# Optimization experiments

Measured on AMD Instinct MI355X. Metric: run time of the kernel, lower is better.

## Reference

```python
import jax, jax.numpy as jnp
import numpy as np

B, T, D = 4, 1024, 1024
H = 16                      # attention heads
DS, DC, EXP = 16, 4, 2      # d_state, d_conv, expand
DIN = EXP * D               # 2048
DTR = D // 16               # dt_rank = 64
TOPK_RATIO = 0.25
EPS = 1e-5


def setup_inputs() -> dict:
    key = jax.random.key(0)
    ks = jax.random.split(key, 16)
    def n(k, shape, scale=0.02):
        return jax.random.normal(k, shape, jnp.float32) * scale
    return {
        "x": jax.random.normal(ks[0], (B, T, D), jnp.float32),
        "ln_w": jnp.ones((D,), jnp.float32),
        "ln_b": jnp.zeros((D,), jnp.float32),
        "r_w1": n(ks[1], (D, D // 2)),
        "r_b1": jnp.zeros((D // 2,), jnp.float32),
        "r_w2": n(ks[2], (D // 2, 1)),
        "r_b2": jnp.zeros((1,), jnp.float32),
        "Wq": n(ks[3], (D, D)), "bq": jnp.zeros((D,), jnp.float32),
        "Wk": n(ks[4], (D, D)), "bk": jnp.zeros((D,), jnp.float32),
        "Wv": n(ks[5], (D, D)), "bv": jnp.zeros((D,), jnp.float32),
        "Wo": n(ks[6], (D, D)), "bo": jnp.zeros((D,), jnp.float32),
        "in_w": n(ks[7], (D, 2 * DIN)),
        "conv_w": n(ks[8], (DIN, DC), 0.1),
        "conv_b": jnp.zeros((DIN,), jnp.float32),
        "xproj_w": n(ks[9], (DIN, DTR + 2 * DS)),
        "dt_w": n(ks[10], (DTR, DIN), 0.1),
        "dt_b": jnp.full((DIN,), -4.0, jnp.float32) + n(ks[11], (DIN,), 0.1),
        "A_log": jnp.log(jnp.broadcast_to(jnp.arange(1, DS + 1, dtype=jnp.float32), (DIN, DS))),
        "Dp": jnp.ones((DIN,), jnp.float32),
        "out_w": n(ks[12], (DIN, D)),
    }


def _attn_core(x, Wq, bq, Wk, bk, Wv, bv, Wo, bo):
    b, L, d = x.shape
    hd = d // H
    q = (x @ Wq + bq).reshape(b, L, H, hd)
    k = (x @ Wk + bk).reshape(b, L, H, hd)
    v = (x @ Wv + bv).reshape(b, L, H, hd)
    scores = jnp.einsum('bqhd,bkhd->bhqk', q, k) / jnp.sqrt(jnp.float32(hd))
    p = jax.nn.softmax(scores, axis=-1)
    o = jnp.einsum('bhqk,bkhd->bqhd', p, v).reshape(b, L, d)
    return o @ Wo + bo


def _ssm_core(u, in_w, conv_w, conv_b, xproj_w, dt_w, dt_b, A_log, Dp, out_w):
    # Mamba-style selective SSM on the sub-sequence u: (b, L, D)
    b, L, _ = u.shape
    xi, z = jnp.split(u @ in_w, 2, axis=-1)            # (b, L, DIN) each
    xp = jnp.pad(xi, ((0, 0), (DC - 1, 0), (0, 0)))    # causal depthwise conv1d
    xc = conv_b + sum(xp[:, j:j + L] * conv_w[:, j] for j in range(DC))
    xc = jax.nn.silu(xc)
    proj = xc @ xproj_w                                # (b, L, DTR + 2*DS)
    dtp = proj[..., :DTR]
    Bm = proj[..., DTR:DTR + DS]
    Cm = proj[..., DTR + DS:]
    delta = jax.nn.softplus(dtp @ dt_w + dt_b)         # (b, L, DIN)
    A = -jnp.exp(A_log)                                # (DIN, DS)
    dA = jnp.exp(delta[..., None] * A)                 # (b, L, DIN, DS)
    dBu = (delta * xc)[..., None] * Bm[:, :, None, :]  # (b, L, DIN, DS)

    def step(h, inp):
        dA_t, dBu_t, C_t = inp
        h = dA_t * h + dBu_t                           # (b, DIN, DS)
        return h, jnp.einsum('bds,bs->bd', h, C_t)

    xs = (jnp.moveaxis(dA, 1, 0), jnp.moveaxis(dBu, 1, 0), jnp.moveaxis(Cm, 1, 0))
    _, ys = jax.lax.scan(step, jnp.zeros((b, DIN, DS), u.dtype), xs)
    y = jnp.moveaxis(ys, 0, 1) + xc * Dp               # (b, L, DIN)
    y = y * jax.nn.silu(z)
    return y @ out_w


def reference(x, ln_w, ln_b, r_w1, r_b1, r_w2, r_b2, Wq, bq, Wk, bk, Wv, bv, Wo, bo,
              in_w, conv_w, conv_b, xproj_w, dt_w, dt_b, A_log, Dp, out_w):
    b, t, d = x.shape
    k = min(max(1, int(TOPK_RATIO * t)), t)            # static top-k count
    # pre-norm (LayerNorm)
    mu = x.mean(-1, keepdims=True)
    var = ((x - mu) ** 2).mean(-1, keepdims=True)
    xn = (x - mu) * jax.lax.rsqrt(var + EPS) * ln_w + ln_b
    # router scores (b, t) and top-k dispatch
    scores = jnp.squeeze(jax.nn.gelu(xn @ r_w1 + r_b1) @ r_w2 + r_b2, -1)
    _, topk_idx = jax.lax.top_k(scores, k)
    bidx = jnp.arange(b)[:, None]
    mask = jnp.zeros((b, t), bool).at[bidx, topk_idx].set(True)
    # unselected positions in ascending order (stable sort of 0/1 mask)
    order = jnp.argsort(mask.astype(jnp.int32), axis=1)
    bottom_idx = order[:, :t - k]
    # SSM branch on bottom (t-k) tokens, order-preserving
    x_ssm = xn[bidx, bottom_idx]                       # (b, t-k, d)
    d_ssm_tok = _ssm_core(x_ssm, in_w, conv_w, conv_b, xproj_w, dt_w, dt_b, A_log, Dp, out_w)
    delta_ssm = jnp.zeros_like(xn).at[bidx, bottom_idx].set(d_ssm_tok)
    # attention branch on top-k tokens only (sparse attention)
    x_attn = xn[bidx, topk_idx]                        # (b, k, d)
    d_attn_tok = _attn_core(x_attn, Wq, bq, Wk, bk, Wv, bv, Wo, bo)
    delta_attn = jnp.zeros_like(xn).at[bidx, topk_idx].set(d_attn_tok)
    # masked merge + residual
    delta = jnp.where(mask[..., None], delta_attn, delta_ssm)
    return x + delta
```

## Files before the change

### kernel.cpp

```cpp
#include <hip/hip_runtime.h>
#include <hip/hip_bf16.h>
#include <cstdint>
#include <cstddef>

typedef unsigned short u16;
typedef __attribute__((ext_vector_type(8))) short short8;
typedef __attribute__((ext_vector_type(4))) float f32x4;

__device__ __forceinline__ float b2f(u16 h){ union{unsigned u; float f;} c; c.u = ((unsigned)h)<<16; return c.f; }
__device__ __forceinline__ u16 f2b(float f){ union{float f; unsigned u;} c; c.f = f; unsigned u = c.u; return (u16)((u + 0x7fffu + ((u>>16)&1u)) >> 16); }
__device__ __forceinline__ float gelu_f(float x){
  float x3 = x*x*x;
  return 0.5f*x*(1.f + tanhf(0.7978845608028654f*(x + 0.044715f*x3)));
}
__device__ __forceinline__ void gload_lds16(const void* g, void* l){
  __builtin_amdgcn_global_load_lds((const __attribute__((address_space(1))) void*)g,
                                   (__attribute__((address_space(3))) void*)l, 16, 0, 0);
}

__global__ __launch_bounds__(256) void k_ln(const float* __restrict__ x, const float* __restrict__ w,
    const float* __restrict__ b, float* __restrict__ xn)
{
  int t = blockIdx.x; int tid = threadIdx.x;
  const float* xr = x + (size_t)t*1024;
  float v0 = xr[tid], v1 = xr[tid+256], v2 = xr[tid+512], v3 = xr[tid+768];
  __shared__ float red[256];
  red[tid] = v0+v1+v2+v3; __syncthreads();
  for (int o=128;o;o>>=1){ if (tid<o) red[tid]+=red[tid+o]; __syncthreads(); }
  float mu = red[0] * (1.f/1024.f);
  __syncthreads();
  float c0=v0-mu,c1=v1-mu,c2=v2-mu,c3=v3-mu;
  red[tid] = c0*c0+c1*c1+c2*c2+c3*c3; __syncthreads();
  for (int o=128;o;o>>=1){ if (tid<o) red[tid]+=red[tid+o]; __syncthreads(); }
  float inv = rsqrtf(red[0]*(1.f/1024.f) + 1e-5f);
  float* xo = xn + (size_t)t*1024;
  xo[tid]     = c0*inv*w[tid]     + b[tid];
  xo[tid+256] = c1*inv*w[tid+256] + b[tid+256];
  xo[tid+512] = c2*inv*w[tid+512] + b[tid+512];
  xo[tid+768] = c3*inv*w[tid+768] + b[tid+768];
}

__global__ __launch_bounds__(256) void k_tcvt(const float* __restrict__ src, u16* __restrict__ dst, int R, int C)
{
  __shared__ float tile[32][33];
  int c0 = blockIdx.x*32, r0 = blockIdx.y*32;
  int lc = threadIdx.x & 31, lr = threadIdx.x >> 5;
  #pragma unroll
  for (int rr=0; rr<4; rr++) tile[lr + rr*8][lc] = src[(size_t)(r0 + lr + rr*8)*C + c0 + lc];
  __syncthreads();
  #pragma unroll
  for (int rr=0; rr<4; rr++) dst[(size_t)(c0 + lr + rr*8)*R + r0 + lc] = f2b(tile[lc][lr + rr*8]);
}

__global__ __launch_bounds__(256) void k_bpack(const float* __restrict__ bq, const float* __restrict__ bk,
    const float* __restrict__ bv, float* __restrict__ o)
{
  int i = blockIdx.x*256 + threadIdx.x;
  o[i] = (i < 1024) ? bq[i] : ((i < 2048) ? bk[i-1024] : bv[i-2048]);
}

__global__ __launch_bounds__(256) void k_gemm_router(const float* __restrict__ A, const float* __restrict__ B,
    const float* __restrict__ bias, float* __restrict__ C, int K, int N)
{
  __shared__ float at[16][64];
  __shared__ float bt[16][68];
  int tid = threadIdx.x;
  int tm = blockIdx.x*64, tn = blockIdx.y*64;
  int tr = tid >> 4, tc = tid & 15;
  float acc[4][4] = {};
  for (int k0=0;k0<K;k0+=16){
    int arow = tid >> 2, ac4 = (tid & 3) * 4;
    float4 va = *(const float4*)&A[(size_t)(tm+arow)*K + k0 + ac4];
    at[ac4+0][arow]=va.x; at[ac4+1][arow]=va.y; at[ac4+2][arow]=va.z; at[ac4+3][arow]=va.w;
    int brow = tid >> 4, bc4 = (tid & 15) * 4;
    *(float4*)&bt[brow][bc4] = *(const float4*)&B[(size_t)(k0+brow)*N + tn + bc4];
    __syncthreads();
    #pragma unroll
    for (int kk=0;kk<16;kk++){
      float a0=at[kk][tr*4+0],a1=at[kk][tr*4+1],a2=at[kk][tr*4+2],a3=at[kk][tr*4+3];
      float b0=bt[kk][tc*4+0],b1=bt[kk][tc*4+1],b2v=bt[kk][tc*4+2],b3=bt[kk][tc*4+3];
      acc[0][0]+=a0*b0; acc[0][1]+=a0*b1; acc[0][2]+=a0*b2v; acc[0][3]+=a0*b3;
      acc[1][0]+=a1*b0; acc[1][1]+=a1*b1; acc[1][2]+=a1*b2v; acc[1][3]+=a1*b3;
      acc[2][0]+=a2*b0; acc[2][1]+=a2*b1; acc[2][2]+=a2*b2v; acc[2][3]+=a2*b3;
      acc[3][0]+=a3*b0; acc[3][1]+=a3*b1; acc[3][2]+=a3*b2v; acc[3][3]+=a3*b3;
    }
    __syncthreads();
  }
  #pragma unroll
  for (int i=0;i<4;i++)
    #pragma unroll
    for (int j=0;j<4;j++){
      int r = tm+tr*4+i, c = tn+tc*4+j;
      C[(size_t)r*N + c] = gelu_f(acc[i][j] + bias[c]);
    }
}

__global__ __launch_bounds__(256) void k_score(const float* __restrict__ h, const float* __restrict__ w2,
    const float* __restrict__ b2, float* __restrict__ scores)
{
  int tok = blockIdx.x*4 + (threadIdx.x >> 6);
  int lane = threadIdx.x & 63;
  const float* hr = h + (size_t)tok*512;
  float s = 0.f;
  #pragma unroll
  for (int i=0;i<8;i++) s += hr[lane + i*64] * w2[lane + i*64];
  #pragma unroll
  for (int o=32;o;o>>=1) s += __shfl_xor(s, o, 64);
  if (lane==0) scores[tok] = s + b2[0];
}

__global__ __launch_bounds__(1024) void k_topk(const float* __restrict__ scores, int* __restrict__ aidx, int* __restrict__ sidx)
{
  int b = blockIdx.x, tid = threadIdx.x;
  __shared__ float s[1024];
  __shared__ int pf[1024];
  s[tid] = scores[b*1024 + tid];
  __syncthreads();
  float my = s[tid];
  int cnt = 0;
  for (int j=0;j<1024;j++){ float sj = s[j]; cnt += (sj > my) || (sj == my && j < tid); }
  int isa = (cnt < 256) ? 1 : 0;
  pf[tid] = isa; __syncthreads();
  for (int o=1;o<1024;o<<=1){
    int add = (tid >= o) ? pf[tid-o] : 0;
    __syncthreads();
    pf[tid] += add;
    __syncthreads();
  }
  int excl = pf[tid] - isa;
  if (isa) aidx[b*256 + excl] = tid;
  else     sidx[b*768 + (tid - excl)] = tid;
}

__global__ __launch_bounds__(256) void k_gather(const float* __restrict__ xn, const int* __restrict__ aidx,
    const int* __restrict__ sidx, u16* __restrict__ xat, u16* __restrict__ xst)
{
  int id = blockIdx.x;
  int b = id >> 10, s = id & 1023;
  int src; u16* dst;
  if (s < 256) { src = aidx[b*256 + s]; dst = xat + (size_t)(b*256 + s)*1024; }
  else { int ss = s - 256; src = sidx[b*768 + ss]; dst = xst + (size_t)(b*768 + ss)*1024; }
  const float* sp = xn + ((size_t)b*1024 + src)*1024;
  int tid = threadIdx.x;
  dst[tid]     = f2b(sp[tid]);
  dst[tid+256] = f2b(sp[tid+256]);
  dst[tid+512] = f2b(sp[tid+512]);
  dst[tid+768] = f2b(sp[tid+768]);
}

template<int BM, int BN>
__global__ __launch_bounds__(256) void k_mfma(const u16* __restrict__ A, int lda,
    const u16* __restrict__ Bt, int ldb, const float* __restrict__ bias,
    float* __restrict__ outf, u16* __restrict__ outb, int M, int N, int K,
    int act, int split)
{
  constexpr int WTM = BM/2, WTN = BN/2;
  constexpr int MI = WTM/16, NJ = WTN/16;
  __shared__ u16 lA[2][BM*32];
  __shared__ u16 lB[2][BN*32];
  const int tid = threadIdx.x;
  const int lane = tid & 63;
  const int wv = tid >> 6;
  const int wm = wv >> 1, wn = wv & 1;
  const int tm = blockIdx.x * BM, tn = blockIdx.y * BN;
  const int r0 = lane & 15;
  const int kg = lane >> 4;

  const int ksl = K / gridDim.z;
  const int kbeg = blockIdx.z * ksl;
  if (gridDim.z > 1) outf += (size_t)blockIdx.z * ((size_t)M * N);

  auto stage = [&](int buf, int kt){
    for (int c = tid; c < BM*4; c += 256) {
      int row = c >> 2, j = c & 3;
      int jj = j ^ ((row >> 1) & 3);
      gload_lds16(&A[(size_t)(tm + row)*lda + kt + jj*8], &lA[buf][c*8]);
    }
    for (int c = tid; c < BN*4; c += 256) {
      int row = c >> 2, j = c & 3;
      int jj = j ^ ((row >> 1) & 3);
      gload_lds16(&Bt[(size_t)(tn + row)*ldb + kt + jj*8], &lB[buf][c*8]);
    }
  };

  f32x4 acc[MI][NJ];
  #pragma unroll
  for (int i=0;i<MI;i++)
    #pragma unroll
    for (int j=0;j<NJ;j++) acc[i][j] = (f32x4){0.f,0.f,0.f,0.f};

  stage(0, kbeg);
  __syncthreads();
  const int nk = ksl / 32;
  int cur = 0;
  for (int t = 0; t < nk; t++) {
    if (t + 1 < nk) stage(cur ^ 1, kbeg + (t+1)*32);
    short8 av[MI], bvv[NJ];
    #pragma unroll
    for (int i=0;i<MI;i++){
      int row = wm*WTM + i*16 + r0;
      av[i] = *(const short8*)&lA[cur][row*32 + ((kg ^ ((row>>1)&3))<<3)];
    }
    #pragma unroll
    for (int j=0;j<NJ;j++){
      int row = wn*WTN + j*16 + r0;
      bvv[j] = *(const short8*)&lB[cur][row*32 + ((kg ^ ((row>>1)&3))<<3)];
    }
    #pragma unroll
    for (int i=0;i<MI;i++)
      #pragma unroll
      for (int j=0;j<NJ;j++)
        acc[i][j] = __builtin_amdgcn_mfma_f32_16x16x32_bf16(av[i], bvv[j], acc[i][j], 0, 0, 0);
    __syncthreads();
    cur ^= 1;
  }

  const int rr = kg * 4;
  #pragma unroll
  for (int i=0;i<MI;i++){
    #pragma unroll
    for (int j=0;j<NJ;j++){
      #pragma unroll
      for (int r=0;r<4;r++){
        int row = tm + wm*WTM + i*16 + rr + r;
        int col = tn + wn*WTN + j*16 + r0;
        float v = acc[i][j][r];
        if (bias) v += bias[col];
        if (act == 1) v = (v > 15.f) ? v : log1pf(__expf(v));
        if (col < split) outf[(size_t)row*split + col] = v;
        else             outb[(size_t)row*(N-split) + (col-split)] = f2b(v);
      }
    }
  }
}

__global__ __launch_bounds__(256) void k_psum(const float* __restrict__ p, float* __restrict__ o)
{
  int i = blockIdx.x*256 + threadIdx.x;
  o[i] = p[i] + p[i+294912] + p[i+589824] + p[i+884736];
}

__global__ __launch_bounds__(256) void k_attn2(const u16* __restrict__ qkv, u16* __restrict__ ob)
{
  __shared__ u16 lKP[16384];
  __shared__ u16 lVt[16384];
  char* KP = (char*)lKP;
  char* VT = (char*)lVt;
  const int tid = threadIdx.x;
  const int lane = tid & 63;
  const int w = tid >> 6;
  const int bx = blockIdx.x;
  const int b = bx >> 6, h = (bx >> 2) & 15, ch = bx & 3;

  const u16* kbase = qkv + (size_t)(b*256)*3072 + 1024 + h*64;
  const u16* vbase = qkv + (size_t)(b*256)*3072 + 2048 + h*64;

  {
    int rr = tid >> 3;
    int c8 = (tid & 7) * 8;
    for (int i = 0; i < 8; i++) {
      int row = i*32 + rr;
      int4 kv = *(const int4*)&kbase[(size_t)row*3072 + c8];
      int koff = row*128 + c8*2;
      *(int4*)(KP + (koff ^ ((row & 7) << 4))) = kv;
      int4 vv = *(const int4*)&vbase[(size_t)row*3072 + c8];
      union { int4 q; u16 u[8]; } vu; vu.q = vv;
      #pragma unroll
      for (int jj = 0; jj < 8; jj++) {
        int j = (jj + rr) & 7;
        int d = c8 + j;
        int voff = d*512 + row*2;
        *(u16*)(VT + (voff ^ ((d & 7) << 4))) = vu.u[j];
      }
    }
  }

  const int r0 = lane & 15;
  const int kg = lane >> 4;
  const int qrow = ch*64 + w*16 + r0;
  const u16* qp = qkv + (size_t)(b*256 + qrow)*3072 + h*64 + kg*8;
  short8 qf0 = *(const short8*)(qp);
  short8 qf1 = *(const short8*)(qp + 32);

  __syncthreads();

  f32x4 acc[16];
  #pragma unroll
  for (int t = 0; t < 16; t++) acc[t] = (f32x4){0.f,0.f,0.f,0.f};
  #pragma unroll
  for (int t = 0; t < 16; t++) {
    int row = t*16 + r0;
    int base = row*128 + kg*16;
    short8 kf0 = *(const short8*)(KP + ((base     ) ^ ((row & 7) << 4)));
    short8 kf1 = *(const short8*)(KP + ((base + 64) ^ ((row & 7) << 4)));
    acc[t] = __builtin_amdgcn_mfma_f32_16x16x32_bf16(qf0, kf0, acc[t], 0, 0, 0);
    acc[t] = __builtin_amdgcn_mfma_f32_16x16x32_bf16(qf1, kf1, acc[t], 0, 0, 0);
  }

  #pragma unroll
  for (int t = 0; t < 16; t++) acc[t] = acc[t] * 0.125f;
  float lsum[4];
  #pragma unroll
  for (int r = 0; r < 4; r++) {
    float mx = -1e30f;
    #pragma unroll
    for (int t = 0; t < 16; t++) mx = fmaxf(mx, acc[t][r]);
    #pragma unroll
    for (int o = 1; o < 16; o <<= 1) mx = fmaxf(mx, __shfl_xor(mx, o, 64));
    float s = 0.f;
    #pragma unroll
    for (int t = 0; t < 16; t++) { float p = __expf(acc[t][r] - mx); acc[t][r] = p; s += p; }
    #pragma unroll
    for (int o = 1; o < 16; o <<= 1) s += __shfl_xor(s, o, 64);
    lsum[r] = s;
  }

  __syncthreads();
  char* PW = KP + w*8192;
  #pragma unroll
  for (int t = 0; t < 16; t++) {
    int col = t*16 + r0;
    #pragma unroll
    for (int r = 0; r < 4; r++) {
      int row = kg*4 + r;
      int off = row*512 + col*2;
      *(u16*)(PW + (off ^ ((row & 7) << 4))) = f2b(acc[t][r]);
    }
  }

  f32x4 oacc[4];
  #pragma unroll
  for (int dt = 0; dt < 4; dt++) oacc[dt] = (f32x4){0.f,0.f,0.f,0.f};
  #pragma unroll
  for (int kc = 0; kc < 8; kc++) {
    int pbase = r0*512 + kc*64 + kg*16;
    short8 pf = *(const short8*)(PW + (pbase ^ ((r0 & 7) << 4)));
    #pragma unroll
    for (int dt = 0; dt < 4; dt++) {
      int vrow = dt*16 + r0;
      int vb2 = vrow*512 + kc*64 + kg*16;
      short8 vf = *(const short8*)(VT + (vb2 ^ ((vrow & 7) << 4)));
      oacc[dt] = __builtin_amdgcn_mfma_f32_16x16x32_bf16(pf, vf, oacc[dt], 0, 0, 0);
    }
  }

  u16* op = ob + (size_t)(b*256 + ch*64 + w*16)*1024 + h*64;
  #pragma unroll
  for (int dt = 0; dt < 4; dt++) {
    #pragma unroll
    for (int r = 0; r < 4; r++) {
      int row = kg*4 + r;
      float v = oacc[dt][r] / lsum[r];
      op[(size_t)row*1024 + dt*16 + r0] = f2b(v);
    }
  }
}

__global__ __launch_bounds__(256) void k_conv(const float* __restrict__ xi, const float* __restrict__ cw,
    const float* __restrict__ cb, float* __restrict__ xc, u16* __restrict__ xcb)
{
  size_t idx = (size_t)blockIdx.x*256 + threadIdx.x;
  int d = (int)(idx & 2047);
  size_t bt = idx >> 11;
  int t = (int)(bt % 768);
  float acc = cb[d];
  const float* p = xi + idx;
  float w0=cw[d*4+0], w1=cw[d*4+1], w2=cw[d*4+2], w3=cw[d*4+3];
  acc += w3 * p[0];
  if (t >= 1) acc += w2 * p[-2048];
  if (t >= 2) acc += w1 * p[-4096];
  if (t >= 3) acc += w0 * p[-6144];
  float sv = acc / (1.f + __expf(-acc));
  xc[idx]  = sv;
  xcb[idx] = f2b(sv);
}

__global__ __launch_bounds__(256) void k_dtp(const float* __restrict__ proj, u16* __restrict__ dtpb)
{
  int idx = blockIdx.x*256 + threadIdx.x;
  int tok = idx >> 6, j = idx & 63;
  dtpb[idx] = f2b(proj[(size_t)tok*96 + j]);
}

__global__ __launch_bounds__(256) void k_scan1(const float* __restrict__ delta, const float* __restrict__ xc,
    const float* __restrict__ proj, const float* __restrict__ A_log, float* __restrict__ cs)
{
  int bid = blockIdx.x;
  int db = bid & 7;
  int c  = (bid >> 3) & 15;
  int b  = bid >> 7;
  int d  = db*256 + threadIdx.x;
  float Ar[16];
  #pragma unroll
  for (int s=0;s<16;s++) Ar[s] = -__expf(A_log[d*16+s]);
  float ap[16], hc[16];
  #pragma unroll
  for (int s=0;s<16;s++){ ap[s]=1.f; hc[s]=0.f; }
  size_t row0 = (size_t)b*768 + c*48;
  for (int t=0;t<48;t++){
    size_t row = row0 + t;
    float dl = delta[row*2048 + d];
    float xv = xc[row*2048 + d];
    float du = dl*xv;
    const float4* bp = (const float4*)&proj[row*96 + 64];
    float4 b0 = bp[0], b1 = bp[1], b2 = bp[2], b3 = bp[3];
    float Bc[16] = {b0.x,b0.y,b0.z,b0.w,b1.x,b1.y,b1.z,b1.w,
                    b2.x,b2.y,b2.z,b2.w,b3.x,b3.y,b3.z,b3.w};
    #pragma unroll
    for (int s=0;s<16;s++){
      float dA = __expf(dl*Ar[s]);
      ap[s] *= dA;
      hc[s] = dA*hc[s] + du*Bc[s];
    }
  }
  size_t base = ((size_t)(b*16 + c)*32)*2048 + d;
  #pragma unroll
  for (int s=0;s<16;s++){
    cs[base + (size_t)s*2048]      = ap[s];
    cs[base + (size_t)(16+s)*2048] = hc[s];
  }
}

__global__ __launch_bounds__(256) void k_scan2(float* __restrict__ cs)
{
  int bid = blockIdx.x;
  int db = bid & 7;
  int s  = (bid >> 3) & 15;
  int b  = bid >> 7;
  int d  = db*256 + threadIdx.x;
  float h = 0.f;
  for (int c=0;c<16;c++){
    size_t base = ((size_t)(b*16 + c)*32)*2048 + d;
    float ap = cs[base + (size_t)s*2048];
    float hc = cs[base + (size_t)(16+s)*2048];
    cs[base + (size_t)(16+s)*2048] = h;
    h = ap*h + hc;
  }
}

__global__ __launch_bounds__(256) void k_scan3(const float* __restrict__ delta, const float* __restrict__ xc,
    const float* __restrict__ proj, const float* __restrict__ cs, const u16* __restrict__ zb,
    const float* __restrict__ A_log, const float* __restrict__ Dp, u16* __restrict__ yb)
{
  int bid = blockIdx.x;
  int db = bid & 7;
  int c  = (bid >> 3) & 15;
  int b  = bid >> 7;
  int d  = db*256 + threadIdx.x;
  float Ar[16];
  #pragma unroll
  for (int s=0;s<16;s++) Ar[s] = -__expf(A_log[d*16+s]);
  float dpv = Dp[d];
  float h[16];
  size_t base = ((size_t)(b*16 + c)*32)*2048 + d;
  #pragma unroll
  for (int s=0;s<16;s++) h[s] = cs[base + (size_t)(16+s)*2048];
  size_t row0 = (size_t)b*768 + c*48;
  for (int t=0;t<48;t++){
    size_t row = row0 + t;
    float dl = delta[row*2048 + d];
    float xv = xc[row*2048 + d];
    float du = dl*xv;
    const float4* bp = (const float4*)&proj[row*96 + 64];
    float4 b0 = bp[0], b1 = bp[1], b2 = bp[2], b3 = bp[3];
    const float4* cp = (const float4*)&proj[row*96 + 80];
    float4 c0 = cp[0], c1 = cp[1], c2 = cp[2], c3 = cp[3];
    float Bc[16] = {b0.x,b0.y,b0.z,b0.w,b1.x,b1.y,b1.z,b1.w,
                    b2.x,b2.y,b2.z,b2.w,b3.x,b3.y,b3.z,b3.w};
    float Cc[16] = {c0.x,c0.y,c0.z,c0.w,c1.x,c1.y,c1.z,c1.w,
                    c2.x,c2.y,c2.z,c2.w,c3.x,c3.y,c3.z,c3.w};
    float y = 0.f;
    #pragma unroll
    for (int s=0;s<16;s++){
      float dA = __expf(dl*Ar[s]);
      h[s] = dA*h[s] + du*Bc[s];
      y += h[s]*Cc[s];
    }
    y += xv*dpv;
    float z = b2f(zb[row*2048 + d]);
    float g = z / (1.f + __expf(-z));
    yb[row*2048 + d] = f2b(y*g);
  }
}

__global__ __launch_bounds__(256) void k_scat(const float* __restrict__ x, const int* __restrict__ idxarr,
    const float* __restrict__ dlt, float* __restrict__ out, int per_b)
{
  int id = blockIdx.x;
  int b = id / per_b;
  int t = idxarr[id];
  const float* xp = x + ((size_t)b*1024 + t)*1024;
  const float* dp = dlt + (size_t)id*1024;
  float* op = out + ((size_t)b*1024 + t)*1024;
  int tid = threadIdx.x;
  op[tid]     = xp[tid]     + dp[tid];
  op[tid+256] = xp[tid+256] + dp[tid+256];
  op[tid+512] = xp[tid+512] + dp[tid+512];
  op[tid+768] = xp[tid+768] + dp[tid+768];
}

extern "C" void kernel_launch(void* const* d_in, const int* in_sizes, int n_in,
                              void* d_out, int out_size, void* d_ws, size_t ws_size,
                              hipStream_t stream)
{
  const float* x      = (const float*)d_in[0];
  const float* ln_w   = (const float*)d_in[1];
  const float* ln_b   = (const float*)d_in[2];
  const float* r_w1   = (const float*)d_in[3];
  const float* r_b1   = (const float*)d_in[4];
  const float* r_w2   = (const float*)d_in[5];
  const float* r_b2   = (const float*)d_in[6];
  const float* Wq     = (const float*)d_in[7];
  const float* bq     = (const float*)d_in[8];
  const float* Wk     = (const float*)d_in[9];
  const float* bk     = (const float*)d_in[10];
  const float* Wv     = (const float*)d_in[11];
  const float* bv     = (const float*)d_in[12];
  const float* Wo     = (const float*)d_in[13];
  const float* bo     = (const float*)d_in[14];
  const float* in_w   = (const float*)d_in[15];
  const float* conv_w = (const float*)d_in[16];
  const float* conv_b = (const float*)d_in[17];
  const float* xproj_w= (const float*)d_in[18];
  const float* dt_w   = (const float*)d_in[19];
  const float* dt_b   = (const float*)d_in[20];
  const float* A_log  = (const float*)d_in[21];
  const float* Dp     = (const float*)d_in[22];
  const float* out_w  = (const float*)d_in[23];
  float* out = (float*)d_out;

  uint8_t* ws = (uint8_t*)d_ws;
  size_t off = 0;
  auto alloc = [&](size_t bytes)->uint8_t*{
    uint8_t* p = ws + off;
    off += (bytes + 255) & ~(size_t)255;
    return p;
  };

  float* xn    = (float*)alloc(4096ull*1024*4);
  u16*   wqt   = (u16*)  alloc(1024ull*1024*2);
  u16*   wkt   = (u16*)  alloc(1024ull*1024*2);
  u16*   wvt   = (u16*)  alloc(1024ull*1024*2);
  u16*   wot   = (u16*)  alloc(1024ull*1024*2);
  u16*   inwt  = (u16*)  alloc(4096ull*1024*2);
  u16*   outwt = (u16*)  alloc(1024ull*2048*2);
  u16*   xpwt  = (u16*)  alloc(96ull*2048*2);
  u16*   dtwt  = (u16*)  alloc(2048ull*64*2);
  float* scores= (float*)alloc(4096*4);
  int*   aidx  = (int*)  alloc(1024*4);
  int*   sidx  = (int*)  alloc(3072*4);
  u16*   xat   = (u16*)  alloc(1024ull*1024*2);
  u16*   xst   = (u16*)  alloc(3072ull*1024*2);
  float* qkvb  = (float*)alloc(3072*4);

  float* s_projp = xn;
  float* cs = xn;

  uint8_t* arena = ws + off;
  float* h = (float*)arena;
  u16*   qkvbuf = (u16*)(arena);
  u16*   obuf   = (u16*)(arena + 6291456);
  float* adelta = (float*)(arena + 8388608);
  float* s_xi   = (float*)(arena);
  u16*   s_zb   = (u16*)(arena + 25165824);
  float* s_xc   = (float*)(arena + 37748736);
  u16*   s_xcb  = (u16*)(arena + 62914560);
  float* s_proj = (float*)(arena + 75497472);
  u16*   s_dtpb = (u16*)(arena + 76677120);
  float* s_delta  = s_xi;
  u16*   s_yb     = s_xcb;
  float* s_sdelta = (float*)s_zb;

  hipLaunchKernelGGL(k_ln, dim3(4096), dim3(256), 0, stream, x, ln_w, ln_b, xn);
  hipLaunchKernelGGL(k_tcvt, dim3(32,32),  dim3(256), 0, stream, Wq,     wqt,   1024, 1024);
  hipLaunchKernelGGL(k_tcvt, dim3(32,32),  dim3(256), 0, stream, Wk,     wkt,   1024, 1024);
  hipLaunchKernelGGL(k_tcvt, dim3(32,32),  dim3(256), 0, stream, Wv,     wvt,   1024, 1024);
  hipLaunchKernelGGL(k_tcvt, dim3(32,32),  dim3(256), 0, stream, Wo,     wot,   1024, 1024);
  hipLaunchKernelGGL(k_tcvt, dim3(128,32), dim3(256), 0, stream, in_w,   inwt,  1024, 4096);
  hipLaunchKernelGGL(k_tcvt, dim3(32,64),  dim3(256), 0, stream, out_w,  outwt, 2048, 1024);
  hipLaunchKernelGGL(k_tcvt, dim3(3,64),   dim3(256), 0, stream, xproj_w,xpwt,  2048, 96);
  hipLaunchKernelGGL(k_tcvt, dim3(64,2),   dim3(256), 0, stream, dt_w,   dtwt,  64,   2048);
  hipLaunchKernelGGL(k_bpack, dim3(12), dim3(256), 0, stream, bq, bk, bv, qkvb);
  hipLaunchKernelGGL(k_gemm_router, dim3(64,8), dim3(256), 0, stream, xn, r_w1, r_b1, h, 1024, 512);
  hipLaunchKernelGGL(k_score, dim3(1024), dim3(256), 0, stream, h, r_w2, r_b2, scores);
  hipLaunchKernelGGL(k_topk, dim3(4), dim3(1024), 0, stream, scores, aidx, sidx);
  hipLaunchKernelGGL(k_gather, dim3(4096), dim3(256), 0, stream, xn, aidx, sidx, xat, xst);
  hipLaunchKernelGGL((k_mfma<64,128>), dim3(16,24), dim3(256), 0, stream,
      xat, 1024, wqt, 1024, qkvb, (float*)nullptr, qkvbuf, 1024, 3072, 1024, 0, 0);
  hipLaunchKernelGGL(k_attn2, dim3(256), dim3(256), 0, stream, qkvbuf, obuf);
  hipLaunchKernelGGL((k_mfma<64,64>), dim3(16,16), dim3(256), 0, stream,
      obuf, 1024, wot, 1024, bo, adelta, (u16*)nullptr, 1024, 1024, 1024, 0, 1024);
  hipLaunchKernelGGL(k_scat, dim3(1024), dim3(256), 0, stream, x, aidx, adelta, out, 256);
  hipLaunchKernelGGL((k_mfma<128,128>), dim3(24,32), dim3(256), 0, stream,
      xst, 1024, inwt, 1024, (const float*)nullptr, s_xi, s_zb, 3072, 4096, 1024, 0, 2048);
  hipLaunchKernelGGL(k_conv, dim3(24576), dim3(256), 0, stream, s_xi, conv_w, conv_b, s_xc, s_xcb);
  hipLaunchKernelGGL((k_mfma<64,96>), dim3(48,1,4), dim3(256), 0, stream,
      s_xcb, 2048, xpwt, 2048, (const float*)nullptr, s_projp, (u16*)nullptr, 3072, 96, 2048, 0, 96);
  hipLaunchKernelGGL(k_psum, dim3(1152), dim3(256), 0, stream, s_projp, s_proj);
  hipLaunchKernelGGL(k_dtp, dim3(768), dim3(256), 0, stream, s_proj, s_dtpb);
  hipLaunchKernelGGL((k_mfma<128,128>), dim3(24,16), dim3(256), 0, stream,
      s_dtpb, 64, dtwt, 64, dt_b, s_delta, (u16*)nullptr, 3072, 2048, 64, 1, 2048);
  hipLaunchKernelGGL(k_scan1, dim3(512), dim3(256), 0, stream, s_delta, s_xc, s_proj, A_log, cs);
  hipLaunchKernelGGL(k_scan2, dim3(512), dim3(256), 0, stream, cs);
  hipLaunchKernelGGL(k_scan3, dim3(512), dim3(256), 0, stream, s_delta, s_xc, s_proj, cs, s_zb, A_log, Dp, s_yb);
  hipLaunchKernelGGL((k_mfma<64,128>), dim3(48,8), dim3(256), 0, stream,
      s_yb, 2048, outwt, 2048, (const float*)nullptr, s_sdelta, (u16*)nullptr, 3072, 1024, 2048, 0, 1024);
  hipLaunchKernelGGL(k_scat, dim3(3072), dim3(256), 0, stream, x, sidx, s_sdelta, out, 768);
}
```

Measured before the change: 477.9 us.

## Route router GEMM through split-bf16 MFMA and vectorize elementwise kernels

The FP32 scalar router GEMM is replaced by a bf16 MFMA GEMM. Both operands are split into hi/lo bf16 parts and concatenated along K (hi*hi + hi*lo + lo*hi) so accuracy stays near FP32 for the top-k selection, and GELU is fused into the GEMM epilogue. LayerNorm switches to float4 loads with wave-shuffle reductions, gather and scatter become float4-vectorized, and the dt-projection bf16 conversion is folded into k_psum so k_dtp can be dropped. The split GEMM triples K and adds two packing kernels plus extra workspace traffic. Any precision loss could still change top-k routing decisions.

```diff
diff --git a/kernel.cpp b/kernel.cpp
--- a/kernel.cpp
+++ b/kernel.cpp
@@ -21,23 +21,26 @@
 __global__ __launch_bounds__(256) void k_ln(const float* __restrict__ x, const float* __restrict__ w,
     const float* __restrict__ b, float* __restrict__ xn)
 {
-  int t = blockIdx.x; int tid = threadIdx.x;
-  const float* xr = x + (size_t)t*1024;
-  float v0 = xr[tid], v1 = xr[tid+256], v2 = xr[tid+512], v3 = xr[tid+768];
-  __shared__ float red[256];
-  red[tid] = v0+v1+v2+v3; __syncthreads();
-  for (int o=128;o;o>>=1){ if (tid<o) red[tid]+=red[tid+o]; __syncthreads(); }
-  float mu = red[0] * (1.f/1024.f);
-  __syncthreads();
-  float c0=v0-mu,c1=v1-mu,c2=v2-mu,c3=v3-mu;
-  red[tid] = c0*c0+c1*c1+c2*c2+c3*c3; __syncthreads();
-  for (int o=128;o;o>>=1){ if (tid<o) red[tid]+=red[tid+o]; __syncthreads(); }
-  float inv = rsqrtf(red[0]*(1.f/1024.f) + 1e-5f);
-  float* xo = xn + (size_t)t*1024;
-  xo[tid]     = c0*inv*w[tid]     + b[tid];
-  xo[tid+256] = c1*inv*w[tid+256] + b[tid+256];
-  xo[tid+512] = c2*inv*w[tid+512] + b[tid+512];
-  xo[tid+768] = c3*inv*w[tid+768] + b[tid+768];
+  int t = blockIdx.x, tid = threadIdx.x;
+  float4 v = ((const float4*)(x + (size_t)t*1024))[tid];
+  float s = v.x+v.y+v.z+v.w;
+  #pragma unroll
+  for (int o=32;o;o>>=1) s += __shfl_xor(s,o,64);
+  __shared__ float r1[4], r2[4];
+  if ((tid&63)==0) r1[tid>>6] = s;
+  __syncthreads();
+  float mu = (r1[0]+r1[1]+r1[2]+r1[3]) * (1.f/1024.f);
+  float4 c = {v.x-mu, v.y-mu, v.z-mu, v.w-mu};
+  float q = c.x*c.x+c.y*c.y+c.z*c.z+c.w*c.w;
+  #pragma unroll
+  for (int o=32;o;o>>=1) q += __shfl_xor(q,o,64);
+  if ((tid&63)==0) r2[tid>>6] = q;
+  __syncthreads();
+  float inv = rsqrtf((r2[0]+r2[1]+r2[2]+r2[3])*(1.f/1024.f) + 1e-5f);
+  float4 wv = ((const float4*)w)[tid];
+  float4 bv = ((const float4*)b)[tid];
+  float4 o4 = {c.x*inv*wv.x+bv.x, c.y*inv*wv.y+bv.y, c.z*inv*wv.z+bv.z, c.w*inv*wv.w+bv.w};
+  ((float4*)(xn + (size_t)t*1024))[tid] = o4;
 }
 
 __global__ __launch_bounds__(256) void k_tcvt(const float* __restrict__ src, u16* __restrict__ dst, int R, int C)
@@ -59,40 +62,34 @@
   o[i] = (i < 1024) ? bq[i] : ((i < 2048) ? bk[i-1024] : bv[i-2048]);
 }
 
-__global__ __launch_bounds__(256) void k_gemm_router(const float* __restrict__ A, const float* __restrict__ B,
-    const float* __restrict__ bias, float* __restrict__ C, int K, int N)
-{
-  __shared__ float at[16][64];
-  __shared__ float bt[16][68];
-  int tid = threadIdx.x;
-  int tm = blockIdx.x*64, tn = blockIdx.y*64;
-  int tr = tid >> 4, tc = tid & 15;
-  float acc[4][4] = {};
-  for (int k0=0;k0<K;k0+=16){
-    int arow = tid >> 2, ac4 = (tid & 3) * 4;
-    float4 va = *(const float4*)&A[(size_t)(tm+arow)*K + k0 + ac4];
-    at[ac4+0][arow]=va.x; at[ac4+1][arow]=va.y; at[ac4+2][arow]=va.z; at[ac4+3][arow]=va.w;
-    int brow = tid >> 4, bc4 = (tid & 15) * 4;
-    *(float4*)&bt[brow][bc4] = *(const float4*)&B[(size_t)(k0+brow)*N + tn + bc4];
-    __syncthreads();
-    #pragma unroll
-    for (int kk=0;kk<16;kk++){
-      float a0=at[kk][tr*4+0],a1=at[kk][tr*4+1],a2=at[kk][tr*4+2],a3=at[kk][tr*4+3];
-      float b0=bt[kk][tc*4+0],b1=bt[kk][tc*4+1],b2v=bt[kk][tc*4+2],b3=bt[kk][tc*4+3];
-      acc[0][0]+=a0*b0; acc[0][1]+=a0*b1; acc[0][2]+=a0*b2v; acc[0][3]+=a0*b3;
-      acc[1][0]+=a1*b0; acc[1][1]+=a1*b1; acc[1][2]+=a1*b2v; acc[1][3]+=a1*b3;
-      acc[2][0]+=a2*b0; acc[2][1]+=a2*b1; acc[2][2]+=a2*b2v; acc[2][3]+=a2*b3;
-      acc[3][0]+=a3*b0; acc[3][1]+=a3*b1; acc[3][2]+=a3*b2v; acc[3][3]+=a3*b3;
-    }
-    __syncthreads();
-  }
-  #pragma unroll
-  for (int i=0;i<4;i++)
-    #pragma unroll
-    for (int j=0;j<4;j++){
-      int r = tm+tr*4+i, c = tn+tc*4+j;
-      C[(size_t)r*N + c] = gelu_f(acc[i][j] + bias[c]);
-    }
+__global__ __launch_bounds__(256) void k_splitA(const float* __restrict__ xn, u16* __restrict__ ap)
+{
+  int id = blockIdx.x*256 + threadIdx.x;
+  int t = id >> 10, k = id & 1023;
+  float x = xn[id];
+  u16 hi = f2b(x);
+  u16 lo = f2b(x - b2f(hi));
+  u16* row = ap + (size_t)t*3072;
+  row[k] = hi; row[1024+k] = hi; row[2048+k] = lo;
+}
+
+__global__ __launch_bounds__(256) void k_splitB(const float* __restrict__ w1, u16* __restrict__ bp)
+{
+  __shared__ float tile[32][33];
+  int n0 = blockIdx.x*32, k0 = blockIdx.y*32;
+  int lc = threadIdx.x & 31, lr = threadIdx.x >> 5;
+  #pragma unroll
+  for (int rr=0; rr<4; rr++) tile[lr+rr*8][lc] = w1[(size_t)(k0+lr+rr*8)*512 + n0+lc];
+  __syncthreads();
+  #pragma unroll
+  for (int rr=0; rr<4; rr++){
+    int n = n0 + lr + rr*8, k = k0 + lc;
+    float x = tile[lc][lr+rr*8];
+    u16 hi = f2b(x);
+    u16 lo = f2b(x - b2f(hi));
+    u16* row = bp + (size_t)n*3072;
+    row[k] = hi; row[1024+k] = lo; row[2048+k] = hi;
+  }
 }
 
 __global__ __launch_bounds__(256) void k_score(const float* __restrict__ h, const float* __restrict__ w2,
@@ -140,12 +137,12 @@
   int src; u16* dst;
   if (s < 256) { src = aidx[b*256 + s]; dst = xat + (size_t)(b*256 + s)*1024; }
   else { int ss = s - 256; src = sidx[b*768 + ss]; dst = xst + (size_t)(b*768 + ss)*1024; }
-  const float* sp = xn + ((size_t)b*1024 + src)*1024;
+  const float4* sp = (const float4*)(xn + ((size_t)b*1024 + src)*1024);
   int tid = threadIdx.x;
-  dst[tid]     = f2b(sp[tid]);
-  dst[tid+256] = f2b(sp[tid+256]);
-  dst[tid+512] = f2b(sp[tid+512]);
-  dst[tid+768] = f2b(sp[tid+768]);
+  float4 vv = sp[tid];
+  union { u16 u[4]; uint2 d; } pk;
+  pk.u[0]=f2b(vv.x); pk.u[1]=f2b(vv.y); pk.u[2]=f2b(vv.z); pk.u[3]=f2b(vv.w);
+  ((uint2*)dst)[tid] = pk.d;
 }
 
 template<int BM, int BN>
@@ -227,6 +224,7 @@
         float v = acc[i][j][r];
         if (bias) v += bias[col];
         if (act == 1) v = (v > 15.f) ? v : log1pf(__expf(v));
+        else if (act == 2) v = gelu_f(v);
         if (col < split) outf[(size_t)row*split + col] = v;
         else             outb[(size_t)row*(N-split) + (col-split)] = f2b(v);
       }
@@ -234,10 +232,14 @@
   }
 }
 
-__global__ __launch_bounds__(256) void k_psum(const float* __restrict__ p, float* __restrict__ o)
+__global__ __launch_bounds__(256) void k_psum(const float* __restrict__ p, float* __restrict__ o,
+    u16* __restrict__ dtpb)
 {
   int i = blockIdx.x*256 + threadIdx.x;
-  o[i] = p[i] + p[i+294912] + p[i+589824] + p[i+884736];
+  float v = p[i] + p[i+294912] + p[i+589824] + p[i+884736];
+  o[i] = v;
+  int tok = i / 96, col = i - tok*96;
+  if (col < 64) dtpb[tok*64 + col] = f2b(v);
 }
 
 __global__ __launch_bounds__(256) void k_attn2(const u16* __restrict__ qkv, u16* __restrict__ ob)
@@ -375,13 +377,6 @@
   xcb[idx] = f2b(sv);
 }
 
-__global__ __launch_bounds__(256) void k_dtp(const float* __restrict__ proj, u16* __restrict__ dtpb)
-{
-  int idx = blockIdx.x*256 + threadIdx.x;
-  int tok = idx >> 6, j = idx & 63;
-  dtpb[idx] = f2b(proj[(size_t)tok*96 + j]);
-}
-
 __global__ __launch_bounds__(256) void k_scan1(const float* __restrict__ delta, const float* __restrict__ xc,
     const float* __restrict__ proj, const float* __restrict__ A_log, float* __restrict__ cs)
 {
@@ -489,14 +484,12 @@
   int id = blockIdx.x;
   int b = id / per_b;
   int t = idxarr[id];
-  const float* xp = x + ((size_t)b*1024 + t)*1024;
-  const float* dp = dlt + (size_t)id*1024;
-  float* op = out + ((size_t)b*1024 + t)*1024;
+  const float4* xp = (const float4*)(x + ((size_t)b*1024 + t)*1024);
+  const float4* dp = (const float4*)(dlt + (size_t)id*1024);
+  float4* op = (float4*)(out + ((size_t)b*1024 + t)*1024);
   int tid = threadIdx.x;
-  op[tid]     = xp[tid]     + dp[tid];
-  op[tid+256] = xp[tid+256] + dp[tid+256];
-  op[tid+512] = xp[tid+512] + dp[tid+512];
-  op[tid+768] = xp[tid+768] + dp[tid+768];
+  float4 a = xp[tid], d = dp[tid];
+  op[tid] = (float4){a.x+d.x, a.y+d.y, a.z+d.z, a.w+d.w};
 }
 
 extern "C" void kernel_launch(void* const* d_in, const int* in_sizes, int n_in,
@@ -546,6 +539,7 @@
   u16*   outwt = (u16*)  alloc(1024ull*2048*2);
   u16*   xpwt  = (u16*)  alloc(96ull*2048*2);
   u16*   dtwt  = (u16*)  alloc(2048ull*64*2);
+  u16*   r1pk  = (u16*)  alloc(512ull*3072*2);
   float* scores= (float*)alloc(4096*4);
   int*   aidx  = (int*)  alloc(1024*4);
   int*   sidx  = (int*)  alloc(3072*4);
@@ -557,7 +551,8 @@
   float* cs = xn;
 
   uint8_t* arena = ws + off;
-  float* h = (float*)arena;
+  float* h  = (float*)arena;
+  u16*   apk = (u16*)(arena + 8388608);
   u16*   qkvbuf = (u16*)(arena);
   u16*   obuf   = (u16*)(arena + 6291456);
   float* adelta = (float*)(arena + 8388608);
@@ -581,7 +576,10 @@
   hipLaunchKernelGGL(k_tcvt, dim3(3,64),   dim3(256), 0, stream, xproj_w,xpwt,  2048, 96);
   hipLaunchKernelGGL(k_tcvt, dim3(64,2),   dim3(256), 0, stream, dt_w,   dtwt,  64,   2048);
   hipLaunchKernelGGL(k_bpack, dim3(12), dim3(256), 0, stream, bq, bk, bv, qkvb);
-  hipLaunchKernelGGL(k_gemm_router, dim3(64,8), dim3(256), 0, stream, xn, r_w1, r_b1, h, 1024, 512);
+  hipLaunchKernelGGL(k_splitB, dim3(16,32), dim3(256), 0, stream, r_w1, r1pk);
+  hipLaunchKernelGGL(k_splitA, dim3(16384), dim3(256), 0, stream, xn, apk);
+  hipLaunchKernelGGL((k_mfma<64,128>), dim3(64,4), dim3(256), 0, stream,
+      apk, 3072, r1pk, 3072, r_b1, h, (u16*)nullptr, 4096, 512, 3072, 2, 512);
   hipLaunchKernelGGL(k_score, dim3(1024), dim3(256), 0, stream, h, r_w2, r_b2, scores);
   hipLaunchKernelGGL(k_topk, dim3(4), dim3(1024), 0, stream, scores, aidx, sidx);
   hipLaunchKernelGGL(k_gather, dim3(4096), dim3(256), 0, stream, xn, aidx, sidx, xat, xst);
@@ -596,8 +594,7 @@
   hipLaunchKernelGGL(k_conv, dim3(24576), dim3(256), 0, stream, s_xi, conv_w, conv_b, s_xc, s_xcb);
   hipLaunchKernelGGL((k_mfma<64,96>), dim3(48,1,4), dim3(256), 0, stream,
       s_xcb, 2048, xpwt, 2048, (const float*)nullptr, s_projp, (u16*)nullptr, 3072, 96, 2048, 0, 96);
-  hipLaunchKernelGGL(k_psum, dim3(1152), dim3(256), 0, stream, s_projp, s_proj);
-  hipLaunchKernelGGL(k_dtp, dim3(768), dim3(256), 0, stream, s_proj, s_dtpb);
+  hipLaunchKernelGGL(k_psum, dim3(1152), dim3(256), 0, stream, s_projp, s_proj, s_dtpb);
   hipLaunchKernelGGL((k_mfma<128,128>), dim3(24,16), dim3(256), 0, stream,
       s_dtpb, 64, dtwt, 64, dt_b, s_delta, (u16*)nullptr, 3072, 2048, 64, 1, 2048);
   hipLaunchKernelGGL(k_scan1, dim3(512), dim3(256), 0, stream, s_delta, s_xc, s_proj, A_log, cs);
```

New measurement: 492.4 us. +3.1%, slower.
